# Performance work log

Hardware: AMD Instinct MI355X
Metric: run time of the kernel (lower is better)

The kernel has to match this reference:

```python
import jax, jax.numpy as jnp
import numpy as np

N = 8192
IN_DIM = 256
HID = 256
OUT_DIM = 256
P_DIM = 3
SIGMA = 1.0


def setup_inputs() -> dict:
    key = jax.random.key(0)
    ks = jax.random.split(key, 7)
    s_in = 1.0 / np.sqrt(IN_DIM)
    inp = {
        "X": jax.random.normal(ks[0], (N, IN_DIM + P_DIM), dtype=jnp.float32),
        "WQ": jax.random.uniform(ks[1], (IN_DIM, HID), jnp.float32, -s_in, s_in),
        "bQ": jax.random.uniform(ks[2], (HID,), jnp.float32, -s_in, s_in),
        "WK": jax.random.uniform(ks[3], (IN_DIM, HID), jnp.float32, -s_in, s_in),
        "bK": jax.random.uniform(ks[4], (HID,), jnp.float32, -s_in, s_in),
        "WV": jax.random.uniform(ks[5], (IN_DIM, OUT_DIM), jnp.float32, -s_in, s_in),
        "bV": jax.random.uniform(ks[6], (OUT_DIM,), jnp.float32, -s_in, s_in),
    }
    return inp


def _softmax_one(x):
    # exp(x - max) / (1 + sum(exp(x - max))) -- faithful to the torch softmax_one
    m = jnp.max(x, axis=-1, keepdims=True)
    e = jnp.exp(x - m)
    return e / (1.0 + jnp.sum(e, axis=-1, keepdims=True))


def reference(X, WQ, bQ, WK, bK, WV, bV):
    P = X[:, -P_DIM:]            # [N, 3] spatial coords
    Xf = X[:, :-P_DIM]           # [N, IN_DIM] features

    Q = Xf @ WQ + bQ             # [N, HID]
    K = Xf @ WK + bK             # [N, HID]
    V = Xf @ WV + bV             # [N, OUT_DIM]

    scores = (Q @ K.T) / jnp.sqrt(jnp.asarray(HID, Xf.dtype))  # [N, N]

    # squared pairwise distances ||P_i - P_j||^2 (cdist(P,P)**2)
    sq = jnp.sum(P * P, axis=-1)                                # [N]
    d2 = jnp.maximum(sq[:, None] + sq[None, :] - 2.0 * (P @ P.T), 0.0)
    decay = jnp.exp(-d2 / (2.0 * SIGMA ** 2))                   # [N, N]

    A = _softmax_one(scores * decay)                             # [N, N]
    H = A @ V                                                    # [N, OUT_DIM]
    # residual: input_dim == output_dim so res_proj is None
    return H + Xf
```

## Files before the change

kernel.cpp:

```cpp
#include <hip/hip_runtime.h>
#include <hip/hip_bf16.h>
#include <stdint.h>

#define NTOK 8192
#define XSTRIDE 259
#define LOG2E 1.4426950408889634f
#define DECC (-3.4712336270551023f)
#define KSPLIT 4
#define SPLEN (NTOK / KSPLIT)
#define BN 32
#define ITERS (SPLEN / BN)

typedef __bf16 bf16x8 __attribute__((ext_vector_type(8)));
typedef float f32x4 __attribute__((ext_vector_type(4)));
typedef unsigned short u16;

union BF8 { u16 u[8]; bf16x8 v; };
union PB  { uint64_t d[2]; bf16x8 v; };

__device__ __forceinline__ u16 f2bf(float f) {
  uint32_t u = __float_as_uint(f);
  u += 0x7FFFu + ((u >> 16) & 1u);
  return (u16)(u >> 16);
}
__device__ __forceinline__ float bf2f(u16 h) {
  return __uint_as_float(((uint32_t)h) << 16);
}
__device__ __forceinline__ float exp2_hw(float x) {
  float r; asm("v_exp_f32 %0, %1" : "=v"(r) : "v"(x)); return r;
}
template<int CTRL>
__device__ __forceinline__ float dpp_rot(float x) {
  int i = __float_as_int(x);
  int y = __builtin_amdgcn_update_dpp(i, i, CTRL, 0xF, 0xF, false);
  return __int_as_float(y);
}
__device__ __forceinline__ float rowsum16(float x) {
  x += dpp_rot<0x121>(x);
  x += dpp_rot<0x122>(x);
  x += dpp_rot<0x124>(x);
  x += dpp_rot<0x128>(x);
  return x;
}
__device__ __forceinline__ f32x4 mfma16(bf16x8 a, bf16x8 b, f32x4 c) {
  return __builtin_amdgcn_mfma_f32_16x16x32_bf16(a, b, c, 0, 0, 0);
}
__device__ __forceinline__ void async16(const void* g, void* l) {
  __builtin_amdgcn_global_load_lds(
      (const __attribute__((address_space(1))) uint32_t*)g,
      (__attribute__((address_space(3))) uint32_t*)l, 16, 0, 0);
}

__global__ void pq_kernel(const float* __restrict__ X, float* __restrict__ pq) {
  int r = blockIdx.x * 256 + threadIdx.x;
  const float* xp = X + (size_t)r * XSTRIDE + 256;
  float x = xp[0], y = xp[1], z = xp[2];
  f32x4 o = { x, y, z, 0.5f * (x * x + y * y + z * z) };
  ((f32x4*)pq)[r] = o;
}

__global__ __launch_bounds__(256) void wprep_kernel(
    const float* __restrict__ WQ, const float* __restrict__ WK,
    const float* __restrict__ WV, u16* __restrict__ Wt) {
  const int o = blockIdx.x;
  const int which = o >> 8, oo = o & 255;
  const float* W = (which == 0) ? WQ : ((which == 1) ? WK : WV);
  const int k = threadIdx.x;
  Wt[(size_t)o * 256 + k] = f2bf(W[(size_t)k * 256 + oo]);
}

__global__ __launch_bounds__(256) void qkv_kernel(
    const float* __restrict__ X, const u16* __restrict__ Wt,
    const float* __restrict__ bQ, const float* __restrict__ bK,
    const float* __restrict__ bV,
    u16* __restrict__ Qb, u16* __restrict__ Kb, u16* __restrict__ Vt) {
  __shared__ u16 wt[64 * 256];
  const int tid = threadIdx.x;
  const int lane = tid & 63;
  const int wave = tid >> 6;
  const int l15 = lane & 15;
  const int q4 = lane >> 4;
  const int rb = blockIdx.x;
  const int ch = blockIdx.y;
  const int which = ch >> 2;
  const int c0 = (ch & 3) * 64;
  const float* bias = (which == 0) ? bQ : ((which == 1) ? bK : bV);

  bf16x8 xa[2][8];
#pragma unroll
  for (int mt = 0; mt < 2; ++mt) {
    const int row = rb * 128 + wave * 32 + mt * 16 + l15;
#pragma unroll
    for (int kc = 0; kc < 8; ++kc) {
      const float* xp = X + (size_t)row * XSTRIDE + kc * 32 + q4 * 8;
      BF8 u;
#pragma unroll
      for (int jj = 0; jj < 8; ++jj) u.u[jj] = f2bf(xp[jj]);
      xa[mt][kc] = u.v;
    }
  }
  {
    const u16* Wsrc = Wt + (size_t)(which * 256 + c0) * 256;
    const int rb0 = wave * 16;
#pragma unroll
    for (int i = 0; i < 8; ++i) {
      int r = rb0 + i * 2 + (lane >> 5);
      int c = (lane & 31) ^ (r & 7);
      async16(Wsrc + (size_t)r * 256 + c * 8, wt + (rb0 + i * 2) * 256);
    }
  }
  asm volatile("s_waitcnt vmcnt(0)" ::: "memory");
  __syncthreads();

  f32x4 acc[2][4];
#pragma unroll
  for (int mt = 0; mt < 2; ++mt)
#pragma unroll
    for (int nt = 0; nt < 4; ++nt) acc[mt][nt] = (f32x4){0.f, 0.f, 0.f, 0.f};

#pragma unroll
  for (int kc = 0; kc < 8; ++kc) {
#pragma unroll
    for (int nt = 0; nt < 4; ++nt) {
      bf16x8 wf = *(const bf16x8*)(wt + (nt * 16 + l15) * 256 +
                                   (((kc * 4 + q4) ^ (l15 & 7)) * 8));
#pragma unroll
      for (int mt = 0; mt < 2; ++mt)
        acc[mt][nt] = mfma16(xa[mt][kc], wf, acc[mt][nt]);
    }
  }
  float bc[4];
#pragma unroll
  for (int nt = 0; nt < 4; ++nt) bc[nt] = bias[c0 + nt * 16 + l15];

#pragma unroll
  for (int mt = 0; mt < 2; ++mt)
#pragma unroll
    for (int nt = 0; nt < 4; ++nt)
#pragma unroll
      for (int r = 0; r < 4; ++r) {
        float v = acc[mt][nt][r] + bc[nt];
        int grow = rb * 128 + wave * 32 + mt * 16 + q4 * 4 + r;
        int gc = c0 + nt * 16 + l15;
        if (which == 2)      Vt[(size_t)gc * NTOK + grow] = f2bf(v);
        else if (which == 1) Kb[(size_t)grow * 256 + gc] = f2bf(v);
        else                 Qb[(size_t)grow * 256 + gc] = f2bf(v);
      }
}

__global__ __launch_bounds__(256, 2) void attn_kernel(
    const u16* __restrict__ Qb, const u16* __restrict__ Kb,
    const u16* __restrict__ Vt, const float* __restrict__ pq,
    u16* __restrict__ Op, float* __restrict__ ml) {
  __shared__ u16 kbuf[2][BN * 256];
  __shared__ u16 vbuf[2][256 * BN];
  __shared__ u16 pbuf[4][16 * 36];
  __shared__ float pqk[2][BN * 4];

  const int tid = threadIdx.x;
  const int lane = tid & 63;
  const int wave = tid >> 6;
  const int l15 = lane & 15;
  const int q4 = lane >> 4;
  const int rb = blockIdx.x;
  const int sp = blockIdx.y;
  const int q0 = rb * 64;
  const int wrow = wave * 16;

#define STAGE(T)                                                              \
  do {                                                                        \
    const int key0_ = sp * SPLEN + (T) * BN;                                  \
    const int b_ = (T) & 1;                                                   \
    if (wave < 2) {                                                           \
      const int rb0 = wave * 16;                                              \
      _Pragma("unroll")                                                       \
      for (int i = 0; i < 8; ++i) {                                           \
        int r = rb0 + i * 2 + (lane >> 5);                                    \
        int c = (lane & 31) ^ (r & 7);                                        \
        async16(Kb + (size_t)(key0_ + r) * 256 + c * 8,                       \
                &kbuf[b_][(rb0 + i * 2) * 256]);                              \
      }                                                                       \
    } else {                                                                  \
      const int fb0 = (wave - 2) * 128;                                       \
      _Pragma("unroll")                                                       \
      for (int i = 0; i < 8; ++i) {                                           \
        int f = fb0 + i * 16 + (lane >> 2);                                   \
        int c = (lane & 3) ^ (f & 3);                                         \
        async16(Vt + (size_t)f * NTOK + key0_ + c * 8,                        \
                &vbuf[b_][(fb0 + i * 16) * 32]);                              \
      }                                                                       \
      if (wave == 3 && lane < 32)                                             \
        async16(((const f32x4*)pq) + key0_ + lane, &pqk[b_][0]);              \
    }                                                                         \
  } while (0)

  bf16x8 qa[8];
#pragma unroll
  for (int kc = 0; kc < 8; ++kc)
    qa[kc] = *(const bf16x8*)(Qb + (size_t)(q0 + wrow + l15) * 256 +
                              kc * 32 + q4 * 8);
  f32x4 pr[4];
#pragma unroll
  for (int r = 0; r < 4; ++r)
    pr[r] = ((const f32x4*)pq)[q0 + wrow + q4 * 4 + r];

  f32x4 O[16];
#pragma unroll
  for (int ft = 0; ft < 16; ++ft) O[ft] = (f32x4){0.f, 0.f, 0.f, 0.f};
  float lrow[4] = {0.f, 0.f, 0.f, 0.f};

  STAGE(0);

#pragma unroll 1
  for (int it = 0; it < ITERS; ++it) {
    const int cur = it & 1;
    asm volatile("s_waitcnt vmcnt(0)" ::: "memory");
    __syncthreads();

    const int nx = (it + 1 < ITERS) ? (it + 1) : (ITERS - 1);
    STAGE(nx);

    f32x4 S[2];
#pragma unroll
    for (int nt = 0; nt < 2; ++nt) S[nt] = (f32x4){0.f, 0.f, 0.f, 0.f};
#pragma unroll
    for (int kc = 0; kc < 8; ++kc) {
#pragma unroll
      for (int nt = 0; nt < 2; ++nt) {
        bf16x8 kf = *(const bf16x8*)(&kbuf[cur][(nt * 16 + l15) * 256 +
                                     (((kc * 4 + q4) ^ (l15 & 7)) * 8)]);
        S[nt] = mfma16(qa[kc], kf, S[nt]);
      }
    }

    {
      f32x4 pk[2];
#pragma unroll
      for (int nt = 0; nt < 2; ++nt)
        pk[nt] = ((const f32x4*)pqk[cur])[nt * 16 + l15];
#pragma unroll
      for (int r = 0; r < 4; ++r) {
        float lacc = 0.f;
#pragma unroll
        for (int nt = 0; nt < 2; ++nt) {
          float h = pr[r][3] + pk[nt][3];
          h = fmaf(-pr[r][0], pk[nt][0], h);
          h = fmaf(-pr[r][1], pk[nt][1], h);
          h = fmaf(-pr[r][2], pk[nt][2], h);
          h = fmaxf(h, 0.f);
          float dec = exp2_hw(fmaf(h, -LOG2E, DECC));
          float p = exp2_hw(S[nt][r] * dec);
          S[nt][r] = p;
          lacc += p;
        }
        lrow[r] += lacc;
      }
    }

    asm volatile("" ::: "memory");
#pragma unroll
    for (int nt = 0; nt < 2; ++nt)
#pragma unroll
      for (int r = 0; r < 4; ++r)
        pbuf[wave][(q4 * 4 + r) * 36 + nt * 16 + l15] = f2bf(S[nt][r]);
    asm volatile("s_waitcnt lgkmcnt(0)" ::: "memory");
    asm volatile("" ::: "memory");

    {
      PB pb;
      const u16* pp = &pbuf[wave][l15 * 36 + q4 * 8];
      pb.d[0] = *(const uint64_t*)(pp);
      pb.d[1] = *(const uint64_t*)(pp + 4);
      bf16x8 pa = pb.v;
#pragma unroll
      for (int ft = 0; ft < 16; ++ft) {
        bf16x8 vf = *(const bf16x8*)(&vbuf[cur][(ft * 16 + l15) * 32 +
                                     ((q4 ^ (l15 & 3)) * 8)]);
        O[ft] = mfma16(pa, vf, O[ft]);
      }
    }
  }

#pragma unroll
  for (int r = 0; r < 4; ++r) lrow[r] = rowsum16(lrow[r]);

#pragma unroll
  for (int ft = 0; ft < 16; ++ft)
#pragma unroll
    for (int r = 0; r < 4; ++r) {
      int row = q0 + wrow + q4 * 4 + r;
      Op[((size_t)sp * NTOK + row) * 256 + ft * 16 + l15] = f2bf(O[ft][r]);
    }
  if (l15 == 0) {
#pragma unroll
    for (int r = 0; r < 4; ++r) {
      int row = q0 + wrow + q4 * 4 + r;
      ml[sp * NTOK + row] = lrow[r];
    }
  }
#undef STAGE
}

__global__ __launch_bounds__(256) void combine_kernel(
    const float* __restrict__ X, const u16* __restrict__ Op,
    const float* __restrict__ ml, float* __restrict__ out) {
  const int row = blockIdx.x;
  const int f = threadIdx.x;
  float den = 1.f, num = 0.f;
#pragma unroll
  for (int s = 0; s < KSPLIT; ++s) {
    den += ml[s * NTOK + row];
    num += bf2f(Op[((size_t)s * NTOK + row) * 256 + f]);
  }
  out[(size_t)row * 256 + f] = num / den + X[(size_t)row * XSTRIDE + f];
}

extern "C" void kernel_launch(void* const* d_in, const int* in_sizes, int n_in,
                              void* d_out, int out_size, void* d_ws, size_t ws_size,
                              hipStream_t stream) {
  (void)in_sizes; (void)n_in; (void)out_size; (void)ws_size;
  const float* X  = (const float*)d_in[0];
  const float* WQ = (const float*)d_in[1];
  const float* bQ = (const float*)d_in[2];
  const float* WK = (const float*)d_in[3];
  const float* bK = (const float*)d_in[4];
  const float* WV = (const float*)d_in[5];
  const float* bV = (const float*)d_in[6];
  float* out = (float*)d_out;
  char* ws = (char*)d_ws;

  u16*   Qb = (u16*)(ws);
  u16*   Kb = (u16*)(ws + ((size_t)4 << 20));
  u16*   Vt = (u16*)(ws + ((size_t)8 << 20));
  float* pq = (float*)(ws + ((size_t)12 << 20));
  u16*   Wt = (u16*)(ws + ((size_t)12 << 20) + 131072);
  u16*   Op = (u16*)(ws + ((size_t)12 << 20) + 131072 + 393216);
  float* ml = (float*)(ws + ((size_t)12 << 20) + 131072 + 393216 +
                       (size_t)KSPLIT * NTOK * 256 * 2);

  pq_kernel<<<dim3(NTOK / 256), dim3(256), 0, stream>>>(X, pq);
  wprep_kernel<<<dim3(768), dim3(256), 0, stream>>>(WQ, WK, WV, Wt);
  qkv_kernel<<<dim3(64, 12), dim3(256), 0, stream>>>(X, Wt, bQ, bK, bV,
                                                     Qb, Kb, Vt);
  attn_kernel<<<dim3(128, KSPLIT), dim3(256), 0, stream>>>(Qb, Kb, Vt, pq,
                                                           Op, ml);
  combine_kernel<<<dim3(NTOK), dim3(256), 0, stream>>>(X, Op, ml, out);
}
```

Before: 200.3 us.

## Switch attention to 32x32 MFMA with register-resident P via permlane swap

Rewrites the attention inner loop to use 32x32x16 bf16 MFMA with 32 query rows per wave. S is computed transposed (K as the A operand), so P can be packed with cvt_pk_bf16 and v_permlane32_swap and fed straight into the PV MFMA with no LDS round trip. Q is pre-laid out in MFMA fragment order by the QKV kernel. The key split is doubled to 8 and the grid is reordered. The changes cut LDS traffic and the fragment shuffle but raise register pressure from a 128-float O accumulator, and the clamp on negative d2 was dropped.

```diff
diff --git a/kernel.cpp b/kernel.cpp
--- a/kernel.cpp
+++ b/kernel.cpp
@@ -6,17 +6,18 @@
 #define XSTRIDE 259
 #define LOG2E 1.4426950408889634f
 #define DECC (-3.4712336270551023f)
-#define KSPLIT 4
+#define KSPLIT 8
 #define SPLEN (NTOK / KSPLIT)
 #define BN 32
 #define ITERS (SPLEN / BN)
 
 typedef __bf16 bf16x8 __attribute__((ext_vector_type(8)));
 typedef float f32x4 __attribute__((ext_vector_type(4)));
+typedef float f32x16 __attribute__((ext_vector_type(16)));
 typedef unsigned short u16;
 
 union BF8 { u16 u[8]; bf16x8 v; };
-union PB  { uint64_t d[2]; bf16x8 v; };
+union PW  { uint32_t u[4]; bf16x8 v; };
 
 __device__ __forceinline__ u16 f2bf(float f) {
   uint32_t u = __float_as_uint(f);
@@ -29,21 +30,11 @@
 __device__ __forceinline__ float exp2_hw(float x) {
   float r; asm("v_exp_f32 %0, %1" : "=v"(r) : "v"(x)); return r;
 }
-template<int CTRL>
-__device__ __forceinline__ float dpp_rot(float x) {
-  int i = __float_as_int(x);
-  int y = __builtin_amdgcn_update_dpp(i, i, CTRL, 0xF, 0xF, false);
-  return __int_as_float(y);
-}
-__device__ __forceinline__ float rowsum16(float x) {
-  x += dpp_rot<0x121>(x);
-  x += dpp_rot<0x122>(x);
-  x += dpp_rot<0x124>(x);
-  x += dpp_rot<0x128>(x);
-  return x;
-}
 __device__ __forceinline__ f32x4 mfma16(bf16x8 a, bf16x8 b, f32x4 c) {
   return __builtin_amdgcn_mfma_f32_16x16x32_bf16(a, b, c, 0, 0, 0);
+}
+__device__ __forceinline__ f32x16 mfma32(bf16x8 a, bf16x8 b, f32x16 c) {
+  return __builtin_amdgcn_mfma_f32_32x32x16_bf16(a, b, c, 0, 0, 0);
 }
 __device__ __forceinline__ void async16(const void* g, void* l) {
   __builtin_amdgcn_global_load_lds(
@@ -144,7 +135,9 @@
         int gc = c0 + nt * 16 + l15;
         if (which == 2)      Vt[(size_t)gc * NTOK + grow] = f2bf(v);
         else if (which == 1) Kb[(size_t)grow * 256 + gc] = f2bf(v);
-        else                 Qb[(size_t)grow * 256 + gc] = f2bf(v);
+        else                 Qb[(size_t)((grow >> 5) * 16 + (gc >> 4)) * 512 +
+                                ((gc >> 3) & 1) * 256 + (grow & 31) * 8 +
+                                (gc & 7)] = f2bf(v);
       }
 }
 
@@ -154,18 +147,17 @@
     u16* __restrict__ Op, float* __restrict__ ml) {
   __shared__ u16 kbuf[2][BN * 256];
   __shared__ u16 vbuf[2][256 * BN];
-  __shared__ u16 pbuf[4][16 * 36];
-  __shared__ float pqk[2][BN * 4];
+  __shared__ __align__(16) float pqk[2][BN * 4];
 
   const int tid = threadIdx.x;
   const int lane = tid & 63;
   const int wave = tid >> 6;
-  const int l15 = lane & 15;
-  const int q4 = lane >> 4;
-  const int rb = blockIdx.x;
-  const int sp = blockIdx.y;
-  const int q0 = rb * 64;
-  const int wrow = wave * 16;
+  const int l31 = lane & 31;
+  const int h5 = lane >> 5;
+  const int sp = blockIdx.x;
+  const int rb = blockIdx.y;
+  const int q0 = rb * 128;
+  const int wrow = wave * 32;
 
 #define STAGE(T)                                                              \
   do {                                                                        \
@@ -180,34 +172,38 @@
         async16(Kb + (size_t)(key0_ + r) * 256 + c * 8,                       \
                 &kbuf[b_][(rb0 + i * 2) * 256]);                              \
       }                                                                       \
+      if (wave == 1 && lane < 32)                                             \
+        async16(((const f32x4*)pq) + key0_ + lane, &pqk[b_][0]);              \
     } else {                                                                  \
       const int fb0 = (wave - 2) * 128;                                       \
       _Pragma("unroll")                                                       \
       for (int i = 0; i < 8; ++i) {                                           \
         int f = fb0 + i * 16 + (lane >> 2);                                   \
-        int c = (lane & 3) ^ (f & 3);                                         \
+        int c = (lane & 3) ^ ((f >> 1) & 3);                                  \
         async16(Vt + (size_t)f * NTOK + key0_ + c * 8,                        \
                 &vbuf[b_][(fb0 + i * 16) * 32]);                              \
       }                                                                       \
-      if (wave == 3 && lane < 32)                                             \
-        async16(((const f32x4*)pq) + key0_ + lane, &pqk[b_][0]);              \
     }                                                                         \
   } while (0)
 
-  bf16x8 qa[8];
-#pragma unroll
-  for (int kc = 0; kc < 8; ++kc)
-    qa[kc] = *(const bf16x8*)(Qb + (size_t)(q0 + wrow + l15) * 256 +
-                              kc * 32 + q4 * 8);
-  f32x4 pr[4];
-#pragma unroll
-  for (int r = 0; r < 4; ++r)
-    pr[r] = ((const f32x4*)pq)[q0 + wrow + q4 * 4 + r];
-
-  f32x4 O[16];
-#pragma unroll
-  for (int ft = 0; ft < 16; ++ft) O[ft] = (f32x4){0.f, 0.f, 0.f, 0.f};
-  float lrow[4] = {0.f, 0.f, 0.f, 0.f};
+  const int rb32 = rb * 4 + wave;
+  bf16x8 qa[16];
+#pragma unroll
+  for (int kc = 0; kc < 16; ++kc)
+    qa[kc] = *(const bf16x8*)(Qb + ((size_t)(rb32 * 16 + kc) * 64 + lane) * 8);
+
+  f32x4 prv = ((const f32x4*)pq)[q0 + wrow + l31];
+  const float nprx = -prv[0], npry = -prv[1], nprz = -prv[2], prw = prv[3];
+
+  f32x16 O[8];
+#pragma unroll
+  for (int ft = 0; ft < 8; ++ft)
+#pragma unroll
+    for (int r = 0; r < 16; ++r) O[ft][r] = 0.f;
+  float lrow = 0.f;
+
+  const int kswz = l31 & 7;
+  const int vswz = (l31 >> 1) & 3;
 
   STAGE(0);
 
@@ -220,84 +216,68 @@
     const int nx = (it + 1 < ITERS) ? (it + 1) : (ITERS - 1);
     STAGE(nx);
 
-    f32x4 S[2];
-#pragma unroll
-    for (int nt = 0; nt < 2; ++nt) S[nt] = (f32x4){0.f, 0.f, 0.f, 0.f};
-#pragma unroll
-    for (int kc = 0; kc < 8; ++kc) {
-#pragma unroll
-      for (int nt = 0; nt < 2; ++nt) {
-        bf16x8 kf = *(const bf16x8*)(&kbuf[cur][(nt * 16 + l15) * 256 +
-                                     (((kc * 4 + q4) ^ (l15 & 7)) * 8)]);
-        S[nt] = mfma16(qa[kc], kf, S[nt]);
+    f32x16 S;
+#pragma unroll
+    for (int r = 0; r < 16; ++r) S[r] = 0.f;
+#pragma unroll
+    for (int kc = 0; kc < 16; ++kc) {
+      bf16x8 kf = *(const bf16x8*)(&kbuf[cur][l31 * 256 +
+                                   (((2 * kc + h5) ^ kswz) * 8)]);
+      S = mfma32(kf, qa[kc], S);
+    }
+
+#pragma unroll
+    for (int r = 0; r < 16; ++r) {
+      f32x4 pk = ((const f32x4*)pqk[cur])[(r & 3) + 8 * (r >> 2) + 4 * h5];
+      float t = pk[3] + prw;
+      t = fmaf(nprx, pk[0], t);
+      t = fmaf(npry, pk[1], t);
+      t = fmaf(nprz, pk[2], t);
+      float dec = exp2_hw(fmaf(t, -LOG2E, DECC));
+      float p = exp2_hw(S[r] * dec);
+      S[r] = p;
+      lrow += p;
+    }
+
+    uint32_t w0, w1, w2, w3, w4, w5, w6, w7;
+    asm("v_cvt_pk_bf16_f32 %0, %1, %2" : "=v"(w0) : "v"(S[0]),  "v"(S[1]));
+    asm("v_cvt_pk_bf16_f32 %0, %1, %2" : "=v"(w1) : "v"(S[2]),  "v"(S[3]));
+    asm("v_cvt_pk_bf16_f32 %0, %1, %2" : "=v"(w2) : "v"(S[4]),  "v"(S[5]));
+    asm("v_cvt_pk_bf16_f32 %0, %1, %2" : "=v"(w3) : "v"(S[6]),  "v"(S[7]));
+    asm("v_cvt_pk_bf16_f32 %0, %1, %2" : "=v"(w4) : "v"(S[8]),  "v"(S[9]));
+    asm("v_cvt_pk_bf16_f32 %0, %1, %2" : "=v"(w5) : "v"(S[10]), "v"(S[11]));
+    asm("v_cvt_pk_bf16_f32 %0, %1, %2" : "=v"(w6) : "v"(S[12]), "v"(S[13]));
+    asm("v_cvt_pk_bf16_f32 %0, %1, %2" : "=v"(w7) : "v"(S[14]), "v"(S[15]));
+    asm volatile("v_permlane32_swap_b32 %0, %1" : "+v"(w2), "+v"(w0));
+    asm volatile("v_permlane32_swap_b32 %0, %1" : "+v"(w3), "+v"(w1));
+    asm volatile("v_permlane32_swap_b32 %0, %1" : "+v"(w6), "+v"(w4));
+    asm volatile("v_permlane32_swap_b32 %0, %1" : "+v"(w7), "+v"(w5));
+    PW pa0, pa1;
+    pa0.u[0] = w0; pa0.u[1] = w1; pa0.u[2] = w2; pa0.u[3] = w3;
+    pa1.u[0] = w4; pa1.u[1] = w5; pa1.u[2] = w6; pa1.u[3] = w7;
+
+#pragma unroll
+    for (int kh = 0; kh < 2; ++kh) {
+      const bf16x8 pa = kh ? pa1.v : pa0.v;
+#pragma unroll
+      for (int ft = 0; ft < 8; ++ft) {
+        bf16x8 vf = *(const bf16x8*)(&vbuf[cur][(ft * 32 + l31) * 32 +
+                                     (((2 * kh + h5) ^ vswz) * 8)]);
+        O[ft] = mfma32(pa, vf, O[ft]);
       }
     }
-
-    {
-      f32x4 pk[2];
-#pragma unroll
-      for (int nt = 0; nt < 2; ++nt)
-        pk[nt] = ((const f32x4*)pqk[cur])[nt * 16 + l15];
-#pragma unroll
-      for (int r = 0; r < 4; ++r) {
-        float lacc = 0.f;
-#pragma unroll
-        for (int nt = 0; nt < 2; ++nt) {
-          float h = pr[r][3] + pk[nt][3];
-          h = fmaf(-pr[r][0], pk[nt][0], h);
-          h = fmaf(-pr[r][1], pk[nt][1], h);
-          h = fmaf(-pr[r][2], pk[nt][2], h);
-          h = fmaxf(h, 0.f);
-          float dec = exp2_hw(fmaf(h, -LOG2E, DECC));
-          float p = exp2_hw(S[nt][r] * dec);
-          S[nt][r] = p;
-          lacc += p;
-        }
-        lrow[r] += lacc;
-      }
-    }
-
-    asm volatile("" ::: "memory");
-#pragma unroll
-    for (int nt = 0; nt < 2; ++nt)
-#pragma unroll
-      for (int r = 0; r < 4; ++r)
-        pbuf[wave][(q4 * 4 + r) * 36 + nt * 16 + l15] = f2bf(S[nt][r]);
-    asm volatile("s_waitcnt lgkmcnt(0)" ::: "memory");
-    asm volatile("" ::: "memory");
-
-    {
-      PB pb;
-      const u16* pp = &pbuf[wave][l15 * 36 + q4 * 8];
-      pb.d[0] = *(const uint64_t*)(pp);
-      pb.d[1] = *(const uint64_t*)(pp + 4);
-      bf16x8 pa = pb.v;
-#pragma unroll
-      for (int ft = 0; ft < 16; ++ft) {
-        bf16x8 vf = *(const bf16x8*)(&vbuf[cur][(ft * 16 + l15) * 32 +
-                                     ((q4 ^ (l15 & 3)) * 8)]);
-        O[ft] = mfma16(pa, vf, O[ft]);
-      }
-    }
-  }
-
-#pragma unroll
-  for (int r = 0; r < 4; ++r) lrow[r] = rowsum16(lrow[r]);
-
-#pragma unroll
-  for (int ft = 0; ft < 16; ++ft)
-#pragma unroll
-    for (int r = 0; r < 4; ++r) {
-      int row = q0 + wrow + q4 * 4 + r;
-      Op[((size_t)sp * NTOK + row) * 256 + ft * 16 + l15] = f2bf(O[ft][r]);
-    }
-  if (l15 == 0) {
-#pragma unroll
-    for (int r = 0; r < 4; ++r) {
-      int row = q0 + wrow + q4 * 4 + r;
-      ml[sp * NTOK + row] = lrow[r];
-    }
-  }
+  }
+
+  float lsum = lrow + __shfl_xor(lrow, 32);
+#pragma unroll
+  for (int ft = 0; ft < 8; ++ft)
+#pragma unroll
+    for (int r = 0; r < 16; ++r) {
+      int row = q0 + wrow + (r & 3) + 8 * (r >> 2) + 4 * h5;
+      Op[((size_t)sp * NTOK + row) * 256 + ft * 32 + l31] = f2bf(O[ft][r]);
+    }
+  if (lane < 32)
+    ml[sp * NTOK + q0 + wrow + lane] = lsum;
 #undef STAGE
 }
 
@@ -342,7 +322,7 @@
   wprep_kernel<<<dim3(768), dim3(256), 0, stream>>>(WQ, WK, WV, Wt);
   qkv_kernel<<<dim3(64, 12), dim3(256), 0, stream>>>(X, Wt, bQ, bK, bV,
                                                      Qb, Kb, Vt);
-  attn_kernel<<<dim3(128, KSPLIT), dim3(256), 0, stream>>>(Qb, Kb, Vt, pq,
-                                                           Op, ml);
+  attn_kernel<<<dim3(KSPLIT, NTOK / 128), dim3(256), 0, stream>>>(
+      Qb, Kb, Vt, pq, Op, ml);
   combine_kernel<<<dim3(NTOK), dim3(256), 0, stream>>>(X, Op, ml, out);
 }
```

New measurement: 287.6 us. 1.44x slower.
